# Optimization experiments

Hardware: AMD Instinct MI355X
Metric: run time of the kernel (lower is better)

## Reference

```python
import jax, jax.numpy as jnp
import numpy as np

B, L, C_IN, N_STOCKS = 128, 256, 8, 50
EPS = 1e-5
SIG_CH_1 = 14 + 14**2 + 14**3   # 2954 = signature_channels(14, 3)
SIG_CH_2 = 9 + 9**2 + 9**3      # 819  = signature_channels(9, 3)


def _conv1d(x, w, b):
    # x: (B, L, Cin); w: (Cout, Cin, K); 'valid' conv along the stream dim
    y = jax.lax.conv_general_dilated(x, w, window_strides=(1,), padding='VALID',
                                     dimension_numbers=('NWC', 'OIW', 'NWC'))
    return y + b


def _augment(x, convs, include_original, include_time):
    # signatory.Augment: conv stack (kernel K then kernel-1 convs with ReLU in between),
    # optionally concatenated with the truncated original stream and a time channel.
    K = convs[0][0].shape[-1]
    L_out = x.shape[1] - K + 1
    pieces = []
    if include_original:
        pieces.append(x[:, K - 1:, :])
    if include_time:
        t = jnp.linspace(0.0, 1.0, L_out, dtype=x.dtype)
        pieces.append(jnp.broadcast_to(t[None, :, None], (x.shape[0], L_out, 1)))
    h = _conv1d(x, *convs[0])
    for w, b in convs[1:]:
        h = _conv1d(jax.nn.relu(h), w, b)
    pieces.append(h)
    return jnp.concatenate(pieces, axis=2)


def _exp3(v):
    # truncated tensor-algebra exponential of a linear increment v: (B, C)
    l1 = v
    l2 = 0.5 * (v[:, :, None] * v[:, None, :])
    l3 = (v[:, :, None, None] * v[:, None, :, None] * v[:, None, None, :]) * (1.0 / 6.0)
    return l1, l2, l3


def _chen(a, b):
    # Chen's identity: truncated tensor product of two depth-3 signatures
    a1, a2, a3 = a
    b1, b2, b3 = b
    c1 = a1 + b1
    c2 = a2 + b2 + a1[:, :, None] * b1[:, None, :]
    c3 = (a3 + b3 + a1[:, :, None, None] * b2[:, None, :, :]
          + a2[:, :, :, None] * b1[:, None, None, :])
    return c1, c2, c3


def _flat(s):
    l1, l2, l3 = s
    bsz = l1.shape[0]
    return jnp.concatenate([l1, l2.reshape(bsz, -1), l3.reshape(bsz, -1)], axis=1)


def _signature(path, stream):
    # path: (B, L, C) -> depth-3 signature; stream=True returns sig at every step
    dx = path[:, 1:, :] - path[:, :-1, :]      # (B, S, C) increments
    init = _exp3(dx[:, 0])
    xs = jnp.moveaxis(dx[:, 1:, :], 1, 0)      # (S-1, B, C)

    def step(carry, v):
        new = _chen(carry, _exp3(v))
        return new, (_flat(new) if stream else jnp.float32(0.0))

    last, outs = jax.lax.scan(step, init, xs)
    if stream:
        return jnp.concatenate([_flat(init)[:, None, :], jnp.moveaxis(outs, 0, 1)], axis=1)
    return _flat(last)


def setup_inputs() -> dict:
    key = jax.random.key(0)
    ks = jax.random.split(key, 12)
    inp = {
        'x': jax.random.normal(ks[0], (B, L, C_IN), dtype=jnp.float32),
        'bn_gamma': jnp.ones((L,), jnp.float32),
        'bn_beta': jnp.zeros((L,), jnp.float32),
        'a1_w1': 0.05 * jax.random.normal(ks[1], (10, C_IN, 5), jnp.float32),
        'a1_b1': 0.05 * jax.random.normal(ks[2], (10,), jnp.float32),
        'a1_w2': 0.05 * jax.random.normal(ks[3], (5, 10, 1), jnp.float32),
        'a1_b2': 0.05 * jax.random.normal(ks[4], (5,), jnp.float32),
        'a2_w1': 0.005 * jax.random.normal(ks[5], (64, SIG_CH_1, 5), jnp.float32),
        'a2_b1': 0.05 * jax.random.normal(ks[6], (64,), jnp.float32),
        'a2_w2': 0.05 * jax.random.normal(ks[7], (8, 64, 1), jnp.float32),
        'a2_b2': 0.05 * jax.random.normal(ks[8], (8,), jnp.float32),
        'lin_w': 1e-4 * jax.random.normal(ks[9], (N_STOCKS, SIG_CH_2), jnp.float32),
        'lin_b': 1e-4 * jax.random.normal(ks[10], (N_STOCKS,), jnp.float32),
    }
    return inp


def reference(x, bn_gamma, bn_beta, a1_w1, a1_b1, a1_w2, a1_b2,
              a2_w1, a2_b1, a2_w2, a2_b2, lin_w, lin_b):
    # BatchNorm1d(nb_sequence) in training mode: normalize over (batch, channel) dims
    mean = x.mean(axis=(0, 2), keepdims=True)
    var = x.var(axis=(0, 2), keepdims=True)
    h = (x - mean) / jnp.sqrt(var + EPS) * bn_gamma[None, :, None] + bn_beta[None, :, None]
    h = _augment(h, [(a1_w1, a1_b1), (a1_w2, a1_b2)], include_original=True, include_time=True)
    h = _signature(h, stream=True)     # (B, L-5, 2954)
    h = _augment(h, [(a2_w1, a2_b1), (a2_w2, a2_b2)], include_original=False, include_time=True)
    h = _signature(h, stream=False)    # (B, 819)
    out = h @ lin_w.T + lin_b
    return jax.nn.softmax(out, axis=1)
```

## Files before the change

### kernel.cpp

```cpp
#include <hip/hip_runtime.h>
#include <cstdint>
#include <cstddef>


#define BATCH 128
#define LSEQ  256
#define CIN   8
#define L1P   252
#define NS1   251
#define SC1   2954
#define TOUT  247
#define OCH   64
#define SC2   819
#define NSTK  50
#define KFLAT 14770
#define KP    14784
#define NKCH  231

typedef __attribute__((ext_vector_type(8))) short short8;
typedef __attribute__((ext_vector_type(16))) float f32x16;

__device__ __forceinline__ void split8(float4 p, float4 q, uint4& hi, uint4& lo) {
  unsigned u0 = __float_as_uint(p.x), u1 = __float_as_uint(p.y);
  unsigned u2 = __float_as_uint(p.z), u3 = __float_as_uint(p.w);
  unsigned u4 = __float_as_uint(q.x), u5 = __float_as_uint(q.y);
  unsigned u6 = __float_as_uint(q.z), u7 = __float_as_uint(q.w);
  hi.x = __builtin_amdgcn_perm(u1, u0, 0x07060302u);
  hi.y = __builtin_amdgcn_perm(u3, u2, 0x07060302u);
  hi.z = __builtin_amdgcn_perm(u5, u4, 0x07060302u);
  hi.w = __builtin_amdgcn_perm(u7, u6, 0x07060302u);
  float r0 = p.x - __uint_as_float(u0 & 0xFFFF0000u);
  float r1 = p.y - __uint_as_float(u1 & 0xFFFF0000u);
  float r2 = p.z - __uint_as_float(u2 & 0xFFFF0000u);
  float r3 = p.w - __uint_as_float(u3 & 0xFFFF0000u);
  float r4 = q.x - __uint_as_float(u4 & 0xFFFF0000u);
  float r5 = q.y - __uint_as_float(u5 & 0xFFFF0000u);
  float r6 = q.z - __uint_as_float(u6 & 0xFFFF0000u);
  float r7 = q.w - __uint_as_float(u7 & 0xFFFF0000u);
  lo.x = __builtin_amdgcn_perm(__float_as_uint(r1), __float_as_uint(r0), 0x07060302u);
  lo.y = __builtin_amdgcn_perm(__float_as_uint(r3), __float_as_uint(r2), 0x07060302u);
  lo.z = __builtin_amdgcn_perm(__float_as_uint(r5), __float_as_uint(r4), 0x07060302u);
  lo.w = __builtin_amdgcn_perm(__float_as_uint(r7), __float_as_uint(r6), 0x07060302u);
}

__global__ __launch_bounds__(256) void k_bn(const float* __restrict__ x,
                                            const float* __restrict__ gamma,
                                            const float* __restrict__ beta,
                                            float* __restrict__ scale,
                                            float* __restrict__ shift) {
  int l = blockIdx.x, tid = threadIdx.x;
  float s = 0.f, q = 0.f;
#pragma unroll
  for (int p = 0; p < 4; ++p) {
    int e = tid + p * 256;
    int b = e >> 3, c = e & 7;
    float v = x[((size_t)b * LSEQ + l) * CIN + c];
    s += v; q += v * v;
  }
  for (int d = 32; d; d >>= 1) { s += __shfl_xor(s, d); q += __shfl_xor(q, d); }
  __shared__ float ss[4], qq[4];
  int w = tid >> 6;
  if ((tid & 63) == 0) { ss[w] = s; qq[w] = q; }
  __syncthreads();
  if (tid == 0) {
    float S = ss[0] + ss[1] + ss[2] + ss[3];
    float Q = qq[0] + qq[1] + qq[2] + qq[3];
    float mean = S * (1.f / 1024.f);
    float var  = Q * (1.f / 1024.f) - mean * mean;
    float istd = 1.0f / sqrtf(var + 1e-5f);
    float sc = istd * gamma[l];
    scale[l] = sc;
    shift[l] = beta[l] - mean * sc;
  }
}

__global__ __launch_bounds__(256) void k_aug1(const float* __restrict__ x,
                                              const float* __restrict__ scale,
                                              const float* __restrict__ shift,
                                              const float* __restrict__ w1,
                                              const float* __restrict__ b1,
                                              const float* __restrict__ w2,
                                              const float* __restrict__ b2,
                                              float* __restrict__ P1) {
  __shared__ float w1s[400], b1s[10], w2s[50], b2s[5];
  int tid = threadIdx.x;
  for (int i = tid; i < 400; i += 256) w1s[i] = w1[i];
  if (tid < 10) b1s[tid] = b1[tid];
  if (tid < 50) w2s[tid] = w2[tid];
  if (tid < 5)  b2s[tid] = b2[tid];
  __syncthreads();
  int g = blockIdx.x * 256 + tid;
  if (g >= BATCH * L1P) return;
  int b = g / L1P, t = g % L1P;
  float xn[5][8];
#pragma unroll
  for (int k = 0; k < 5; ++k) {
    int l = t + k;
    float sc = scale[l], sh = shift[l];
#pragma unroll
    for (int c = 0; c < 8; ++c)
      xn[k][c] = x[((size_t)b * LSEQ + l) * CIN + c] * sc + sh;
  }
  float r10[10];
#pragma unroll
  for (int co = 0; co < 10; ++co) {
    float s = b1s[co];
#pragma unroll
    for (int c = 0; c < 8; ++c)
#pragma unroll
      for (int k = 0; k < 5; ++k)
        s += xn[k][c] * w1s[co * 40 + c * 5 + k];
    r10[co] = fmaxf(s, 0.f);
  }
  float* o = P1 + ((size_t)b * L1P + t) * 14;
#pragma unroll
  for (int c = 0; c < 8; ++c) o[c] = xn[4][c];
  o[8] = (float)t * (1.0f / 251.0f);
#pragma unroll
  for (int oo = 0; oo < 5; ++oo) {
    float s = b2s[oo];
#pragma unroll
    for (int co = 0; co < 10; ++co) s += r10[co] * w2s[oo * 10 + co];
    o[9 + oo] = s;
  }
}

__global__ __launch_bounds__(256) void k_wtf(const float* __restrict__ w,
                                             float* __restrict__ Wf) {
  int idx = blockIdx.x * 256 + threadIdx.x;
  if (idx >= OCH * KP) return;
  int o = idx / KP, kf = idx % KP;
  float v = 0.f;
  if (kf < KFLAT) {
    int tap = kf / SC1, c = kf % SC1;
    v = w[((size_t)o * SC1 + c) * 5 + tap];
  }
  Wf[idx] = v;
}

__global__ __launch_bounds__(256) void k_scanA(const float* __restrict__ P1,
                                               float* __restrict__ Sw,
                                               int NRbuf, int w0, int RW) {
  int s = blockIdx.x, b = blockIdx.y, tid = threadIdx.x;
  int r0 = s * 16;
  int cnt = RW - r0; if (cnt > 16) cnt = 16;
  if (cnt <= 0) return;
  const float* p = P1 + (size_t)b * L1P * 14 + (size_t)(w0 + r0) * 14;
  float* Sb = Sw + ((size_t)b * NRbuf + r0) * SC1;
  __shared__ float a1s[14], a2s[196], vs[2][14], b2s[2][196];
  float a3[11];
  int ia[11], i2[11], il2[11], ik[11];
#pragma unroll
  for (int n = 0; n < 11; ++n) {
    int e = tid + n * 256;
    ia[n] = e / 196; i2[n] = e / 14; il2[n] = e % 196; ik[n] = e % 14;
  }
  if (tid < 14) vs[0][tid] = p[14 + tid] - p[tid];
  if (tid < 196) {
    int j = tid / 14, k = tid % 14;
    b2s[0][tid] = 0.5f * (p[14 + j] - p[j]) * (p[14 + k] - p[k]);
  }
  __syncthreads();
  for (int j = 0; j < cnt; ++j) {
    int buf = j & 1;
    float c1n = 0.f, c2n = 0.f;
    if (j == 0) {
      if (tid < 14)  c1n = vs[buf][tid];
      if (tid < 196) c2n = b2s[buf][tid];
#pragma unroll
      for (int n = 0; n < 11; ++n) {
        int e = tid + n * 256;
        if (e < 2744) a3[n] = vs[buf][ia[n]] * b2s[buf][il2[n]] * (1.f / 3.f);
      }
    } else {
#pragma unroll
      for (int n = 0; n < 11; ++n) {
        int e = tid + n * 256;
        if (e < 2744)
          a3[n] += (a1s[ia[n]] + vs[buf][ia[n]] * (1.f / 3.f)) * b2s[buf][il2[n]]
                 + a2s[i2[n]] * vs[buf][ik[n]];
      }
      if (tid < 196) c2n = a2s[tid] + b2s[buf][tid] + a1s[tid / 14] * vs[buf][tid % 14];
      if (tid < 14)  c1n = a1s[tid] + vs[buf][tid];
    }
    __syncthreads();
    if (tid < 14)  a1s[tid] = c1n;
    if (tid < 196) a2s[tid] = c2n;
    {
      float* o = Sb + (size_t)j * SC1;
      if (tid < 14)  o[tid] = c1n;
      if (tid < 196) o[14 + tid] = c2n;
#pragma unroll
      for (int n = 0; n < 11; ++n) {
        int e = tid + n * 256;
        if (e < 2744) o[210 + e] = a3[n];
      }
    }
    if (j + 1 < cnt) {
      int nb = buf ^ 1;
      const float* pj = p + (size_t)(j + 1) * 14;
      if (tid < 14) vs[nb][tid] = pj[14 + tid] - pj[tid];
      if (tid < 196) {
        int jj = tid / 14, kk = tid % 14;
        b2s[nb][tid] = 0.5f * (pj[14 + jj] - pj[jj]) * (pj[14 + kk] - pj[kk]);
      }
    }
    __syncthreads();
  }
}

__global__ __launch_bounds__(256) void k_scanB(const float* __restrict__ Sw,
                                               float* __restrict__ Pfx,
                                               float* __restrict__ carry,
                                               int NRbuf, int RW, int NC, int NCC) {
  int b = blockIdx.x, tid = threadIdx.x;
  __shared__ float a1s[14], a2s[196], b1s[14], b2s[196];
  float a3[11], b3[11];
  int ia[11], i2[11], il2[11], ik[11];
#pragma unroll
  for (int n = 0; n < 11; ++n) {
    int e = tid + n * 256;
    ia[n] = e / 196; i2[n] = e / 14; il2[n] = e % 196; ik[n] = e % 14;
  }
  const float* Sb = Sw + (size_t)b * NRbuf * SC1;
  float* cb = carry + (size_t)b * SC1;
  if (tid < 14)  a1s[tid] = cb[tid];
  if (tid < 196) a2s[tid] = cb[14 + tid];
#pragma unroll
  for (int n = 0; n < 11; ++n) { int e = tid + n * 256; if (e < 2744) a3[n] = cb[210 + e]; }
  __syncthreads();
  for (int s = 0; s < NC; ++s) {
    int cnt = RW - s * 16; if (cnt > 16) cnt = 16;
    const float* tr = Sb + (size_t)(s * 16 + cnt - 1) * SC1;
    if (tid < 14)  b1s[tid] = tr[tid];
    if (tid < 196) b2s[tid] = tr[14 + tid];
#pragma unroll
    for (int n = 0; n < 11; ++n) { int e = tid + n * 256; if (e < 2744) b3[n] = tr[210 + e]; }
    __syncthreads();
    float* ps = Pfx + ((size_t)b * 16 + s) * SC1;
    if (tid < 14)  ps[tid] = a1s[tid];
    if (tid < 196) ps[14 + tid] = a2s[tid];
#pragma unroll
    for (int n = 0; n < 11; ++n) { int e = tid + n * 256; if (e < 2744) ps[210 + e] = a3[n]; }
#pragma unroll
    for (int n = 0; n < 11; ++n) {
      int e = tid + n * 256;
      if (e < 2744) a3[n] += b3[n] + a1s[ia[n]] * b2s[il2[n]] + a2s[i2[n]] * b1s[ik[n]];
    }
    float c1n = 0.f, c2n = 0.f;
    if (tid < 196) c2n = a2s[tid] + b2s[tid] + a1s[tid / 14] * b1s[tid % 14];
    if (tid < 14)  c1n = a1s[tid] + b1s[tid];
    __syncthreads();
    if (tid < 14)  a1s[tid] = c1n;
    if (tid < 196) a2s[tid] = c2n;
    if (s == NCC - 1) {
      if (tid < 14)  cb[tid] = c1n;
      if (tid < 196) cb[14 + tid] = c2n;
#pragma unroll
      for (int n = 0; n < 11; ++n) { int e = tid + n * 256; if (e < 2744) cb[210 + e] = a3[n]; }
    }
  }
}

__global__ __launch_bounds__(256) void k_scanC3(float* __restrict__ Sw,
                                                const float* __restrict__ Pfx,
                                                int NRbuf, int RW) {
  int s = blockIdx.x, b = blockIdx.y, tid = threadIdx.x;
  int r0 = s * 16;
  int rows = RW - r0; if (rows > 16) rows = 16;
  if (rows <= 0) return;
  __shared__ float pa[SC1];
  __shared__ float lb[4][216];
  const float* P = Pfx + ((size_t)b * 16 + s) * SC1;
  for (int i = tid; i < SC1; i += 256) pa[i] = P[i];
  __syncthreads();
  int w = tid >> 6, lane = tid & 63;
  float* base = Sw + ((size_t)b * NRbuf + r0) * SC1;
#pragma unroll
  for (int j = 0; j < 4; ++j) {
    int rr = w + j * 4;
    if (rr < rows) {
      float* row = base + (size_t)rr * SC1;
      if (lane < 53) {
        float4 v = *(const float4*)(row + lane * 4);
        *(float4*)&lb[w][lane * 4] = v;
      }
      asm volatile("s_waitcnt lgkmcnt(0)" ::: "memory");
      for (int c = lane; c < SC1; c += 64) {
        float v = row[c];
        float f;
        if (c < 14) {
          f = pa[c] + v;
        } else if (c < 210) {
          int e = c - 14;
          f = pa[c] + v + pa[e / 14] * lb[w][e % 14];
        } else {
          int e = c - 210;
          int i3 = e / 196, rjk = e - i3 * 196;
          int i2 = e / 14,  kk  = e - i2 * 14;
          f = pa[c] + v + pa[i3] * lb[w][14 + rjk] + pa[14 + i2] * lb[w][kk];
        }
        row[c] = f;
      }
    }
  }
}

__global__ __launch_bounds__(256) void k_gemm3(const float* __restrict__ Sw,
                                               const float* __restrict__ Wf,
                                               const float* __restrict__ bias,
                                               float* __restrict__ C1,
                                               int NRbuf, int w0, int WTcur) {
  const int t0 = blockIdx.x * 64;
  const int b  = blockIdx.y;
  const int tid = threadIdx.x, lane = tid & 63;
  __shared__ __align__(16) short Ah[4096], Al[4096], Bh[4096], Bl[4096];
  f32x16 acc;
#pragma unroll
  for (int i = 0; i < 16; ++i) acc[i] = 0.f;

  const float* Sb = Sw + (size_t)b * ((size_t)NRbuf * SC1);
  const int arow = tid >> 2;
  const int g0 = tid & 3, g1 = g0 + 4;
  const int at = min(t0 + arow, WTcur - 1);
  const float* aP = Sb + (size_t)at * SC1;
  const float* bP = Wf + (size_t)arow * KP;
  const int sw = arow & 7;
  const int offA0 = arow * 64 + ((g0 ^ sw) << 3);
  const int offA1 = arow * 64 + ((g1 ^ sw) << 3);
  float4 a0, a1, a2, a3, w0v, w1v, w2v, w3v;

  auto LOADCH = [&](int k0) {
    a0 = *(const float4*)(aP + k0 + g0 * 8);
    a1 = *(const float4*)(aP + k0 + g0 * 8 + 4);
    a2 = *(const float4*)(aP + k0 + g1 * 8);
    a3 = *(const float4*)(aP + k0 + g1 * 8 + 4);
    w0v = *(const float4*)(bP + k0 + g0 * 8);
    w1v = *(const float4*)(bP + k0 + g0 * 8 + 4);
    w2v = *(const float4*)(bP + k0 + g1 * 8);
    w3v = *(const float4*)(bP + k0 + g1 * 8 + 4);
  };
  auto STORECH = [&]() {
    uint4 hi, lo;
    split8(a0, a1, hi, lo);
    *(uint4*)&Ah[offA0] = hi; *(uint4*)&Al[offA0] = lo;
    split8(a2, a3, hi, lo);
    *(uint4*)&Ah[offA1] = hi; *(uint4*)&Al[offA1] = lo;
    split8(w0v, w1v, hi, lo);
    *(uint4*)&Bh[offA0] = hi; *(uint4*)&Bl[offA0] = lo;
    split8(w2v, w3v, hi, lo);
    *(uint4*)&Bh[offA1] = hi; *(uint4*)&Bl[offA1] = lo;
  };

  const int rowA = ((tid >> 6) & 1) * 32 + (lane & 31);
  const int rowB = (tid >> 7) * 32 + (lane & 31);
  const int swA = rowA & 7, swB = rowB & 7;
  const int baseA = rowA * 64, baseB = rowB * 64;

  LOADCH(0);
  STORECH();
  __syncthreads();

  for (int ch = 0; ch < NKCH; ++ch) {
    if (ch + 1 < NKCH) LOADCH((ch + 1) * 64);
#pragma unroll
    for (int ks = 0; ks < 4; ++ks) {
      const int kga = 2 * ks + (lane >> 5);
      const short8 ah = *(const short8*)&Ah[baseA + ((kga ^ swA) << 3)];
      const short8 al = *(const short8*)&Al[baseA + ((kga ^ swA) << 3)];
      const short8 bh = *(const short8*)&Bh[baseB + ((kga ^ swB) << 3)];
      const short8 bl = *(const short8*)&Bl[baseB + ((kga ^ swB) << 3)];
      acc = __builtin_amdgcn_mfma_f32_32x32x16_bf16(ah, bh, acc, 0, 0, 0);
      acc = __builtin_amdgcn_mfma_f32_32x32x16_bf16(ah, bl, acc, 0, 0, 0);
      acc = __builtin_amdgcn_mfma_f32_32x32x16_bf16(al, bh, acc, 0, 0, 0);
    }
    __syncthreads();
    if (ch + 1 < NKCH) { STORECH(); __syncthreads(); }
  }

  const float bia = bias[rowB];
  const int mbase = t0 + ((tid >> 6) & 1) * 32;
#pragma unroll
  for (int q = 0; q < 16; ++q) {
    int crow = (q & 3) + 8 * (q >> 2) + 4 * (lane >> 5);
    int t_l = mbase + crow;
    if (t_l < WTcur)
      C1[((size_t)b * TOUT + w0 + t_l) * OCH + rowB] = acc[q] + bia;
  }
}

__global__ __launch_bounds__(256) void k_p2(const float* __restrict__ C1,
                                            const float* __restrict__ w2,
                                            const float* __restrict__ b2,
                                            float* __restrict__ P2) {
  int warp = blockIdx.x * 4 + (threadIdx.x >> 6);
  int lane = threadIdx.x & 63;
  int b = warp / TOUT, t = warp % TOUT;
  float v = fmaxf(C1[((size_t)b * TOUT + t) * OCH + lane], 0.f);
  float* o = P2 + ((size_t)b * TOUT + t) * 9;
#pragma unroll
  for (int oo = 0; oo < 8; ++oo) {
    float s = v * w2[oo * 64 + lane];
    for (int d = 32; d; d >>= 1) s += __shfl_xor(s, d);
    if (lane == oo) o[1 + oo] = s + b2[oo];
  }
  if (lane == 8) o[0] = (float)t * (1.0f / 246.0f);
}

__global__ __launch_bounds__(256) void k_sig2A(const float* __restrict__ P2,
                                               float* __restrict__ T2) {
  int ch = blockIdx.x, b = blockIdx.y, tid = threadIdx.x;
  int r0 = ch * 16;
  int steps = 246 - r0; if (steps > 16) steps = 16;
  const float* p = P2 + (size_t)b * TOUT * 9;
  __shared__ float a1s[9], a2s[81], vs[2][9], b2s[2][81];
  float a3[3];
  int ia[3], i2[3], il2[3], ik[3];
#pragma unroll
  for (int n = 0; n < 3; ++n) {
    int e = tid + n * 256;
    ia[n] = e / 81; i2[n] = e / 9; il2[n] = e % 81; ik[n] = e % 9;
  }
  {
    int r = r0;
    if (tid < 9) vs[0][tid] = p[(r + 1) * 9 + tid] - p[r * 9 + tid];
    if (tid < 81) {
      int j = tid / 9, k = tid % 9;
      b2s[0][tid] = 0.5f * (p[(r + 1) * 9 + j] - p[r * 9 + j])
                         * (p[(r + 1) * 9 + k] - p[r * 9 + k]);
    }
  }
  __syncthreads();
  for (int s = 0; s < steps; ++s) {
    int buf = s & 1, r = r0 + s;
    float c1n = 0.f, c2n = 0.f;
    if (s == 0) {
      if (tid < 9)  c1n = vs[buf][tid];
      if (tid < 81) c2n = b2s[buf][tid];
#pragma unroll
      for (int n = 0; n < 3; ++n) {
        int e = tid + n * 256;
        if (e < 729) a3[n] = vs[buf][ia[n]] * b2s[buf][il2[n]] * (1.f / 3.f);
      }
    } else {
#pragma unroll
      for (int n = 0; n < 3; ++n) {
        int e = tid + n * 256;
        if (e < 729)
          a3[n] += (a1s[ia[n]] + vs[buf][ia[n]] * (1.f / 3.f)) * b2s[buf][il2[n]]
                 + a2s[i2[n]] * vs[buf][ik[n]];
      }
      if (tid < 81) c2n = a2s[tid] + b2s[buf][tid] + a1s[tid / 9] * vs[buf][tid % 9];
      if (tid < 9)  c1n = a1s[tid] + vs[buf][tid];
    }
    __syncthreads();
    if (tid < 9)  a1s[tid] = c1n;
    if (tid < 81) a2s[tid] = c2n;
    if (s + 1 < steps) {
      int r2 = r + 1, nb = buf ^ 1;
      if (tid < 9) vs[nb][tid] = p[(r2 + 1) * 9 + tid] - p[r2 * 9 + tid];
      if (tid < 81) {
        int j = tid / 9, k = tid % 9;
        b2s[nb][tid] = 0.5f * (p[(r2 + 1) * 9 + j] - p[r2 * 9 + j])
                            * (p[(r2 + 1) * 9 + k] - p[r2 * 9 + k]);
      }
    }
    __syncthreads();
  }
  {
    float* tb = T2 + ((size_t)b * 16 + ch) * SC2;
    if (tid < 9)  tb[tid] = a1s[tid];
    if (tid < 81) tb[9 + tid] = a2s[tid];
#pragma unroll
    for (int n = 0; n < 3; ++n) {
      int e = tid + n * 256;
      if (e < 729) tb[90 + e] = a3[n];
    }
  }
}

__global__ __launch_bounds__(256) void k_sig2B(const float* __restrict__ T2,
                                               float* __restrict__ sg) {
  int b = blockIdx.x, tid = threadIdx.x;
  __shared__ float a1s[9], a2s[81], b1s[9], b2s[81];
  float a3[3], b3[3];
  int ia[3], i2[3], il2[3], ik[3];
#pragma unroll
  for (int n = 0; n < 3; ++n) {
    int e = tid + n * 256;
    ia[n] = e / 81; i2[n] = e / 9; il2[n] = e % 81; ik[n] = e % 9;
  }
  const float* base = T2 + (size_t)b * 16 * SC2;
  if (tid < 9)  a1s[tid] = base[tid];
  if (tid < 81) a2s[tid] = base[9 + tid];
#pragma unroll
  for (int n = 0; n < 3; ++n) { int e = tid + n * 256; if (e < 729) a3[n] = base[90 + e]; }
  __syncthreads();
  for (int ch = 1; ch < 16; ++ch) {
    const float* sl = base + (size_t)ch * SC2;
    if (tid < 9)  b1s[tid] = sl[tid];
    if (tid < 81) b2s[tid] = sl[9 + tid];
#pragma unroll
    for (int n = 0; n < 3; ++n) { int e = tid + n * 256; if (e < 729) b3[n] = sl[90 + e]; }
    __syncthreads();
#pragma unroll
    for (int n = 0; n < 3; ++n) {
      int e = tid + n * 256;
      if (e < 729) a3[n] += b3[n] + a1s[ia[n]] * b2s[il2[n]] + a2s[i2[n]] * b1s[ik[n]];
    }
    float c1n = 0.f, c2n = 0.f;
    if (tid < 81) c2n = a2s[tid] + b2s[tid] + a1s[tid / 9] * b1s[tid % 9];
    if (tid < 9)  c1n = a1s[tid] + b1s[tid];
    __syncthreads();
    if (tid < 9)  a1s[tid] = c1n;
    if (tid < 81) a2s[tid] = c2n;
    __syncthreads();
  }
  float* o = sg + (size_t)b * SC2;
  if (tid < 9)  o[tid] = a1s[tid];
  if (tid < 81) o[9 + tid] = a2s[tid];
#pragma unroll
  for (int n = 0; n < 3; ++n) { int e = tid + n * 256; if (e < 729) o[90 + e] = a3[n]; }
}

__global__ __launch_bounds__(64) void k_final(const float* __restrict__ sg,
                                              const float* __restrict__ lw,
                                              const float* __restrict__ lb,
                                              float* __restrict__ out) {
  int b = blockIdx.x, lane = threadIdx.x;
  float logit = -3.402823466e38f;
  if (lane < NSTK) {
    float s = lb[lane];
    const float* w = lw + (size_t)lane * SC2;
    const float* g = sg + (size_t)b * SC2;
    for (int c = 0; c < SC2; ++c) s += g[c] * w[c];
    logit = s;
  }
  float m = logit;
  for (int d = 32; d; d >>= 1) m = fmaxf(m, __shfl_xor(m, d));
  float e = (lane < NSTK) ? expf(logit - m) : 0.f;
  float sum = e;
  for (int d = 32; d; d >>= 1) sum += __shfl_xor(sum, d);
  if (lane < NSTK) out[(size_t)b * NSTK + lane] = e / sum;
}

extern "C" void kernel_launch(void* const* d_in, const int* in_sizes, int n_in,
                              void* d_out, int out_size, void* d_ws, size_t ws_size,
                              hipStream_t stream) {
  const float* x      = (const float*)d_in[0];
  const float* gamma  = (const float*)d_in[1];
  const float* beta   = (const float*)d_in[2];
  const float* a1w1   = (const float*)d_in[3];
  const float* a1b1   = (const float*)d_in[4];
  const float* a1w2   = (const float*)d_in[5];
  const float* a1b2   = (const float*)d_in[6];
  const float* a2w1   = (const float*)d_in[7];
  const float* a2b1   = (const float*)d_in[8];
  const float* a2w2   = (const float*)d_in[9];
  const float* a2b2   = (const float*)d_in[10];
  const float* lin_w  = (const float*)d_in[11];
  const float* lin_b  = (const float*)d_in[12];
  float* out = (float*)d_out;

  float* ws = (float*)d_ws;
  float* scale = ws;
  float* shift = ws + 256;
  float* P1    = ws + 512;
  float* Wf    = ws + 452096;
  float* carry = ws + 1398272;
  float* Pfx   = ws + 1776384;
  float* P2    = ws + 7826176;
  float* sig2  = ws + 8110720;
  float* C1    = ws + 8215552;
  const size_t off_Swin = 10238976;
  float* Swin  = ws + off_Swin;
  float* T2    = Pfx;

  size_t ws_floats = ws_size / 4;
  long avail = (long)ws_floats - (long)off_Swin - 64;
  long slot = (long)BATCH * SC1;
  int NRbuf = (int)(avail > 0 ? avail / slot : 0);
  if (NRbuf > 251) NRbuf = 251;
  if (NRbuf < 24)  NRbuf = 24;
  int WT = (NRbuf >= 251) ? 247 : ((NRbuf - 4) / 16) * 16;
  int nwin = (TOUT + WT - 1) / WT;

  hipMemsetAsync(carry, 0, (size_t)slot * 4, stream);

  k_bn  <<<LSEQ, 256, 0, stream>>>(x, gamma, beta, scale, shift);
  k_aug1<<<(BATCH * L1P) / 256, 256, 0, stream>>>(x, scale, shift, a1w1, a1b1, a1w2, a1b2, P1);
  k_wtf <<<(OCH * KP) / 256, 256, 0, stream>>>(a2w1, Wf);

  for (int w = 0; w < nwin; ++w) {
    int w0 = w * WT;
    int WTcur = TOUT - w0; if (WTcur > WT) WTcur = WT;
    int RW = WTcur + 4;
    int NC = (RW + 15) / 16;
    int NCC = (w + 1 < nwin) ? (WT / 16) : -2;
    k_scanA<<<dim3(NC, BATCH), 256, 0, stream>>>(P1, Swin, NRbuf, w0, RW);
    k_scanB<<<BATCH, 256, 0, stream>>>(Swin, Pfx, carry, NRbuf, RW, NC, NCC);
    k_scanC3<<<dim3(NC, BATCH), 256, 0, stream>>>(Swin, Pfx, NRbuf, RW);
    int tiles = (WTcur + 63) / 64;
    k_gemm3<<<dim3(tiles, BATCH), 256, 0, stream>>>(Swin, Wf, a2b1, C1, NRbuf, w0, WTcur);
  }

  k_p2   <<<(BATCH * TOUT) / 4, 256, 0, stream>>>(C1, a2w2, a2b2, P2);
  k_sig2A<<<dim3(16, BATCH), 256, 0, stream>>>(P2, T2);
  k_sig2B<<<BATCH, 256, 0, stream>>>(T2, sig2);
  k_final<<<BATCH, 64, 0, stream>>>(sig2, lin_w, lin_b, out);
}
```

Measured before the change: 1.144 ms.

## Pre-pack bf16 hi/lo pairs, use 128x64 tiles with split-K GEMM

The scan epilogue and the weight transform now store each float as a packed 32-bit word holding a bf16 high part and a rounded bf16 residual. The GEMM no longer has to split fp32 into hi/lo inside its loop, and each operand occupies one shared-memory array instead of two. The GEMM is rewritten to use 128x64 tiles with two accumulators per wave and split-K across blocks, writing partial sums that k_p2 reduces and adds the bias to. This is meant to raise parallelism and per-tile reuse, at the cost of extra partial-sum traffic and a larger workspace, which may shrink the window buffer.

```diff
diff --git a/kernel.cpp b/kernel.cpp
--- a/kernel.cpp
+++ b/kernel.cpp
@@ -20,27 +20,13 @@
 typedef __attribute__((ext_vector_type(8))) short short8;
 typedef __attribute__((ext_vector_type(16))) float f32x16;
 
-__device__ __forceinline__ void split8(float4 p, float4 q, uint4& hi, uint4& lo) {
-  unsigned u0 = __float_as_uint(p.x), u1 = __float_as_uint(p.y);
-  unsigned u2 = __float_as_uint(p.z), u3 = __float_as_uint(p.w);
-  unsigned u4 = __float_as_uint(q.x), u5 = __float_as_uint(q.y);
-  unsigned u6 = __float_as_uint(q.z), u7 = __float_as_uint(q.w);
-  hi.x = __builtin_amdgcn_perm(u1, u0, 0x07060302u);
-  hi.y = __builtin_amdgcn_perm(u3, u2, 0x07060302u);
-  hi.z = __builtin_amdgcn_perm(u5, u4, 0x07060302u);
-  hi.w = __builtin_amdgcn_perm(u7, u6, 0x07060302u);
-  float r0 = p.x - __uint_as_float(u0 & 0xFFFF0000u);
-  float r1 = p.y - __uint_as_float(u1 & 0xFFFF0000u);
-  float r2 = p.z - __uint_as_float(u2 & 0xFFFF0000u);
-  float r3 = p.w - __uint_as_float(u3 & 0xFFFF0000u);
-  float r4 = q.x - __uint_as_float(u4 & 0xFFFF0000u);
-  float r5 = q.y - __uint_as_float(u5 & 0xFFFF0000u);
-  float r6 = q.z - __uint_as_float(u6 & 0xFFFF0000u);
-  float r7 = q.w - __uint_as_float(u7 & 0xFFFF0000u);
-  lo.x = __builtin_amdgcn_perm(__float_as_uint(r1), __float_as_uint(r0), 0x07060302u);
-  lo.y = __builtin_amdgcn_perm(__float_as_uint(r3), __float_as_uint(r2), 0x07060302u);
-  lo.z = __builtin_amdgcn_perm(__float_as_uint(r5), __float_as_uint(r4), 0x07060302u);
-  lo.w = __builtin_amdgcn_perm(__float_as_uint(r7), __float_as_uint(r6), 0x07060302u);
+__device__ __forceinline__ unsigned int pack2(float x) {
+  unsigned int u = __float_as_uint(x);
+  unsigned int hi = u >> 16;
+  float rem = x - __uint_as_float(hi << 16);
+  unsigned int v = __float_as_uint(rem);
+  unsigned int lo = (v + 0x7FFFu + ((v >> 16) & 1u)) >> 16;
+  return (hi << 16) | lo;
 }
 
 __global__ __launch_bounds__(256) void k_bn(const float* __restrict__ x,
@@ -125,8 +111,8 @@
   }
 }
 
-__global__ __launch_bounds__(256) void k_wtf(const float* __restrict__ w,
-                                             float* __restrict__ Wf) {
+__global__ __launch_bounds__(256) void k_wtp(const float* __restrict__ w,
+                                             unsigned int* __restrict__ Wp) {
   int idx = blockIdx.x * 256 + threadIdx.x;
   if (idx >= OCH * KP) return;
   int o = idx / KP, kf = idx % KP;
@@ -135,7 +121,7 @@
     int tap = kf / SC1, c = kf % SC1;
     v = w[((size_t)o * SC1 + c) * 5 + tap];
   }
-  Wf[idx] = v;
+  Wp[idx] = pack2(v);
 }
 
 __global__ __launch_bounds__(256) void k_scanA(const float* __restrict__ P1,
@@ -281,6 +267,7 @@
     int rr = w + j * 4;
     if (rr < rows) {
       float* row = base + (size_t)rr * SC1;
+      unsigned int* rowp = (unsigned int*)row;
       if (lane < 53) {
         float4 v = *(const float4*)(row + lane * 4);
         *(float4*)&lb[w][lane * 4] = v;
@@ -300,103 +287,144 @@
           int i2 = e / 14,  kk  = e - i2 * 14;
           f = pa[c] + v + pa[i3] * lb[w][14 + rjk] + pa[14 + i2] * lb[w][kk];
         }
-        row[c] = f;
-      }
-    }
-  }
-}
-
-__global__ __launch_bounds__(256) void k_gemm3(const float* __restrict__ Sw,
-                                               const float* __restrict__ Wf,
-                                               const float* __restrict__ bias,
-                                               float* __restrict__ C1,
-                                               int NRbuf, int w0, int WTcur) {
-  const int t0 = blockIdx.x * 64;
-  const int b  = blockIdx.y;
-  const int tid = threadIdx.x, lane = tid & 63;
-  __shared__ __align__(16) short Ah[4096], Al[4096], Bh[4096], Bl[4096];
-  f32x16 acc;
-#pragma unroll
-  for (int i = 0; i < 16; ++i) acc[i] = 0.f;
-
-  const float* Sb = Sw + (size_t)b * ((size_t)NRbuf * SC1);
-  const int arow = tid >> 2;
-  const int g0 = tid & 3, g1 = g0 + 4;
-  const int at = min(t0 + arow, WTcur - 1);
-  const float* aP = Sb + (size_t)at * SC1;
-  const float* bP = Wf + (size_t)arow * KP;
-  const int sw = arow & 7;
-  const int offA0 = arow * 64 + ((g0 ^ sw) << 3);
-  const int offA1 = arow * 64 + ((g1 ^ sw) << 3);
-  float4 a0, a1, a2, a3, w0v, w1v, w2v, w3v;
-
-  auto LOADCH = [&](int k0) {
-    a0 = *(const float4*)(aP + k0 + g0 * 8);
-    a1 = *(const float4*)(aP + k0 + g0 * 8 + 4);
-    a2 = *(const float4*)(aP + k0 + g1 * 8);
-    a3 = *(const float4*)(aP + k0 + g1 * 8 + 4);
-    w0v = *(const float4*)(bP + k0 + g0 * 8);
-    w1v = *(const float4*)(bP + k0 + g0 * 8 + 4);
-    w2v = *(const float4*)(bP + k0 + g1 * 8);
-    w3v = *(const float4*)(bP + k0 + g1 * 8 + 4);
+        rowp[c] = pack2(f);
+      }
+    }
+  }
+}
+
+__global__ __launch_bounds__(256, 3) void k_gemm4(const unsigned int* __restrict__ Sp,
+                                                  const unsigned int* __restrict__ Wp,
+                                                  float* __restrict__ Cpart,
+                                                  int NRbuf, int w0, int WTcur,
+                                                  int nks, int cpk) {
+  const int mt = blockIdx.x / nks, ksid = blockIdx.x % nks;
+  const int b = blockIdx.y;
+  const int tid = threadIdx.x, lane = tid & 63, w = tid >> 6;
+  __shared__ unsigned int As[128 * 64];
+  __shared__ unsigned int Bs[64 * 64];
+  f32x16 acc0, acc1;
+#pragma unroll
+  for (int i = 0; i < 16; ++i) { acc0[i] = 0.f; acc1[i] = 0.f; }
+
+  const unsigned int* Sb = Sp + (size_t)b * ((size_t)NRbuf * SC1);
+  const int slot = tid & 15;
+  const int rsub = (tid >> 4) & 3;
+  uint4 ra[8], rb[4];
+  const int c0 = ksid * cpk;
+  int c1 = c0 + cpk; if (c1 > NKCH) c1 = NKCH;
+
+  auto GLOAD = [&](int ch) {
+    const int k0 = ch * 64;
+#pragma unroll
+    for (int p = 0; p < 8; ++p) {
+      int rl = w * 32 + p * 4 + rsub;
+      int t = mt * 128 + rl; if (t > WTcur - 1) t = WTcur - 1;
+      ra[p] = *(const uint4*)(Sb + (size_t)t * SC1 + k0 + slot * 4);
+    }
+#pragma unroll
+    for (int p = 0; p < 4; ++p) {
+      int o = w * 16 + p * 4 + rsub;
+      rb[p] = *(const uint4*)(Wp + (size_t)o * KP + k0 + slot * 4);
+    }
   };
-  auto STORECH = [&]() {
-    uint4 hi, lo;
-    split8(a0, a1, hi, lo);
-    *(uint4*)&Ah[offA0] = hi; *(uint4*)&Al[offA0] = lo;
-    split8(a2, a3, hi, lo);
-    *(uint4*)&Ah[offA1] = hi; *(uint4*)&Al[offA1] = lo;
-    split8(w0v, w1v, hi, lo);
-    *(uint4*)&Bh[offA0] = hi; *(uint4*)&Bl[offA0] = lo;
-    split8(w2v, w3v, hi, lo);
-    *(uint4*)&Bh[offA1] = hi; *(uint4*)&Bl[offA1] = lo;
+  auto SSTORE = [&]() {
+#pragma unroll
+    for (int p = 0; p < 8; ++p) {
+      int rl = w * 32 + p * 4 + rsub;
+      *(uint4*)&As[rl * 64 + ((slot ^ (rl & 15)) << 2)] = ra[p];
+    }
+#pragma unroll
+    for (int p = 0; p < 4; ++p) {
+      int o = w * 16 + p * 4 + rsub;
+      *(uint4*)&Bs[o * 64 + ((slot ^ (o & 15)) << 2)] = rb[p];
+    }
   };
 
-  const int rowA = ((tid >> 6) & 1) * 32 + (lane & 31);
-  const int rowB = (tid >> 7) * 32 + (lane & 31);
-  const int swA = rowA & 7, swB = rowB & 7;
-  const int baseA = rowA * 64, baseB = rowB * 64;
-
-  LOADCH(0);
-  STORECH();
-  __syncthreads();
-
-  for (int ch = 0; ch < NKCH; ++ch) {
-    if (ch + 1 < NKCH) LOADCH((ch + 1) * 64);
+  GLOAD(c0);
+  SSTORE();
+  __syncthreads();
+
+  const int rA = w * 32 + (lane & 31);
+  const int cB0 = lane & 31, cB1 = cB0 + 32;
+  const int swA = rA & 15, swB = cB0 & 15;
+  const int hsh = (lane >> 5) << 1;
+
+  union U { unsigned int u[4]; short8 s; };
+
+  for (int ch = c0; ch < c1; ++ch) {
+    if (ch + 1 < c1) GLOAD(ch + 1);
 #pragma unroll
     for (int ks = 0; ks < 4; ++ks) {
-      const int kga = 2 * ks + (lane >> 5);
-      const short8 ah = *(const short8*)&Ah[baseA + ((kga ^ swA) << 3)];
-      const short8 al = *(const short8*)&Al[baseA + ((kga ^ swA) << 3)];
-      const short8 bh = *(const short8*)&Bh[baseB + ((kga ^ swB) << 3)];
-      const short8 bl = *(const short8*)&Bl[baseB + ((kga ^ swB) << 3)];
-      acc = __builtin_amdgcn_mfma_f32_32x32x16_bf16(ah, bh, acc, 0, 0, 0);
-      acc = __builtin_amdgcn_mfma_f32_32x32x16_bf16(ah, bl, acc, 0, 0, 0);
-      acc = __builtin_amdgcn_mfma_f32_32x32x16_bf16(al, bh, acc, 0, 0, 0);
-    }
-    __syncthreads();
-    if (ch + 1 < NKCH) { STORECH(); __syncthreads(); }
-  }
-
-  const float bia = bias[rowB];
-  const int mbase = t0 + ((tid >> 6) & 1) * 32;
+      const int s0 = ks * 4 + hsh;
+      const uint4 aA = *(const uint4*)&As[rA * 64 + ((s0 ^ swA) << 2)];
+      const uint4 aB = *(const uint4*)&As[rA * 64 + (((s0 + 1) ^ swA) << 2)];
+      const uint4 p0 = *(const uint4*)&Bs[cB0 * 64 + ((s0 ^ swB) << 2)];
+      const uint4 p1 = *(const uint4*)&Bs[cB0 * 64 + (((s0 + 1) ^ swB) << 2)];
+      const uint4 q0 = *(const uint4*)&Bs[cB1 * 64 + ((s0 ^ swB) << 2)];
+      const uint4 q1 = *(const uint4*)&Bs[cB1 * 64 + (((s0 + 1) ^ swB) << 2)];
+      U ah, al, b0h, b0l, b1h, b1l;
+      ah.u[0] = __builtin_amdgcn_perm(aA.y, aA.x, 0x07060302u);
+      ah.u[1] = __builtin_amdgcn_perm(aA.w, aA.z, 0x07060302u);
+      ah.u[2] = __builtin_amdgcn_perm(aB.y, aB.x, 0x07060302u);
+      ah.u[3] = __builtin_amdgcn_perm(aB.w, aB.z, 0x07060302u);
+      al.u[0] = __builtin_amdgcn_perm(aA.y, aA.x, 0x05040100u);
+      al.u[1] = __builtin_amdgcn_perm(aA.w, aA.z, 0x05040100u);
+      al.u[2] = __builtin_amdgcn_perm(aB.y, aB.x, 0x05040100u);
+      al.u[3] = __builtin_amdgcn_perm(aB.w, aB.z, 0x05040100u);
+      b0h.u[0] = __builtin_amdgcn_perm(p0.y, p0.x, 0x07060302u);
+      b0h.u[1] = __builtin_amdgcn_perm(p0.w, p0.z, 0x07060302u);
+      b0h.u[2] = __builtin_amdgcn_perm(p1.y, p1.x, 0x07060302u);
+      b0h.u[3] = __builtin_amdgcn_perm(p1.w, p1.z, 0x07060302u);
+      b0l.u[0] = __builtin_amdgcn_perm(p0.y, p0.x, 0x05040100u);
+      b0l.u[1] = __builtin_amdgcn_perm(p0.w, p0.z, 0x05040100u);
+      b0l.u[2] = __builtin_amdgcn_perm(p1.y, p1.x, 0x05040100u);
+      b0l.u[3] = __builtin_amdgcn_perm(p1.w, p1.z, 0x05040100u);
+      b1h.u[0] = __builtin_amdgcn_perm(q0.y, q0.x, 0x07060302u);
+      b1h.u[1] = __builtin_amdgcn_perm(q0.w, q0.z, 0x07060302u);
+      b1h.u[2] = __builtin_amdgcn_perm(q1.y, q1.x, 0x07060302u);
+      b1h.u[3] = __builtin_amdgcn_perm(q1.w, q1.z, 0x07060302u);
+      b1l.u[0] = __builtin_amdgcn_perm(q0.y, q0.x, 0x05040100u);
+      b1l.u[1] = __builtin_amdgcn_perm(q0.w, q0.z, 0x05040100u);
+      b1l.u[2] = __builtin_amdgcn_perm(q1.y, q1.x, 0x05040100u);
+      b1l.u[3] = __builtin_amdgcn_perm(q1.w, q1.z, 0x05040100u);
+      acc0 = __builtin_amdgcn_mfma_f32_32x32x16_bf16(ah.s, b0h.s, acc0, 0, 0, 0);
+      acc0 = __builtin_amdgcn_mfma_f32_32x32x16_bf16(ah.s, b0l.s, acc0, 0, 0, 0);
+      acc0 = __builtin_amdgcn_mfma_f32_32x32x16_bf16(al.s, b0h.s, acc0, 0, 0, 0);
+      acc1 = __builtin_amdgcn_mfma_f32_32x32x16_bf16(ah.s, b1h.s, acc1, 0, 0, 0);
+      acc1 = __builtin_amdgcn_mfma_f32_32x32x16_bf16(ah.s, b1l.s, acc1, 0, 0, 0);
+      acc1 = __builtin_amdgcn_mfma_f32_32x32x16_bf16(al.s, b1h.s, acc1, 0, 0, 0);
+    }
+    __syncthreads();
+    if (ch + 1 < c1) { SSTORE(); __syncthreads(); }
+  }
+
+  const size_t part = ((size_t)ksid * BATCH + b) * TOUT * OCH;
 #pragma unroll
   for (int q = 0; q < 16; ++q) {
     int crow = (q & 3) + 8 * (q >> 2) + 4 * (lane >> 5);
-    int t_l = mbase + crow;
-    if (t_l < WTcur)
-      C1[((size_t)b * TOUT + w0 + t_l) * OCH + rowB] = acc[q] + bia;
-  }
-}
-
-__global__ __launch_bounds__(256) void k_p2(const float* __restrict__ C1,
+    int tl = mt * 128 + w * 32 + crow;
+    if (tl < WTcur) {
+      size_t o = part + (size_t)(w0 + tl) * OCH;
+      Cpart[o + cB0] = acc0[q];
+      Cpart[o + cB1] = acc1[q];
+    }
+  }
+}
+
+__global__ __launch_bounds__(256) void k_p2(const float* __restrict__ Cpart,
+                                            const float* __restrict__ bias,
                                             const float* __restrict__ w2,
                                             const float* __restrict__ b2,
-                                            float* __restrict__ P2) {
+                                            float* __restrict__ P2, int nks) {
   int warp = blockIdx.x * 4 + (threadIdx.x >> 6);
   int lane = threadIdx.x & 63;
   int b = warp / TOUT, t = warp % TOUT;
-  float v = fmaxf(C1[((size_t)b * TOUT + t) * OCH + lane], 0.f);
+  size_t idx = ((size_t)b * TOUT + t) * OCH + lane;
+  const size_t part = (size_t)BATCH * TOUT * OCH;
+  float v = bias[lane];
+  for (int ks = 0; ks < nks; ++ks) v += Cpart[(size_t)ks * part + idx];
+  v = fmaxf(v, 0.f);
   float* o = P2 + ((size_t)b * TOUT + t) * 9;
 #pragma unroll
   for (int oo = 0; oo < 8; ++oo) {
@@ -563,33 +591,42 @@
   float* out = (float*)d_out;
 
   float* ws = (float*)d_ws;
-  float* scale = ws;
-  float* shift = ws + 256;
-  float* P1    = ws + 512;
-  float* Wf    = ws + 452096;
-  float* carry = ws + 1398272;
-  float* Pfx   = ws + 1776384;
-  float* P2    = ws + 7826176;
-  float* sig2  = ws + 8110720;
-  float* C1    = ws + 8215552;
-  const size_t off_Swin = 10238976;
-  float* Swin  = ws + off_Swin;
-  float* T2    = Pfx;
-
+  float*        scale = ws;
+  float*        shift = ws + 256;
+  float*        P1    = ws + 512;
+  unsigned int* Wp    = (unsigned int*)(ws + 452096);
+  float*        carry = ws + 1398272;
+  float*        Pfx   = ws + 1776384;
+  float*        P2    = ws + 7826176;
+  float*        sig2  = ws + 8110720;
+  float*        Cpart = ws + 8215552;
+  float*        T2    = Pfx;
+
+  const size_t PARTSZ = (size_t)BATCH * TOUT * OCH;
   size_t ws_floats = ws_size / 4;
-  long avail = (long)ws_floats - (long)off_Swin - 64;
   long slot = (long)BATCH * SC1;
+
+  int nks = 4;
+  long off_Swin = 0, avail = 0;
+  for (;;) {
+    off_Swin = 8215552 + (long)nks * (long)PARTSZ;
+    avail = (long)ws_floats - off_Swin - 1024;
+    if (nks == 1 || (avail > 0 && avail / slot >= 24)) break;
+    nks >>= 1;
+  }
   int NRbuf = (int)(avail > 0 ? avail / slot : 0);
   if (NRbuf > 251) NRbuf = 251;
   if (NRbuf < 24)  NRbuf = 24;
   int WT = (NRbuf >= 251) ? 247 : ((NRbuf - 4) / 16) * 16;
   int nwin = (TOUT + WT - 1) / WT;
+  int cpk = (NKCH + nks - 1) / nks;
+  float* Swin = ws + off_Swin;
 
   hipMemsetAsync(carry, 0, (size_t)slot * 4, stream);
 
   k_bn  <<<LSEQ, 256, 0, stream>>>(x, gamma, beta, scale, shift);
   k_aug1<<<(BATCH * L1P) / 256, 256, 0, stream>>>(x, scale, shift, a1w1, a1b1, a1w2, a1b2, P1);
-  k_wtf <<<(OCH * KP) / 256, 256, 0, stream>>>(a2w1, Wf);
+  k_wtp <<<(OCH * KP) / 256, 256, 0, stream>>>(a2w1, Wp);
 
   for (int w = 0; w < nwin; ++w) {
     int w0 = w * WT;
@@ -600,11 +637,12 @@
     k_scanA<<<dim3(NC, BATCH), 256, 0, stream>>>(P1, Swin, NRbuf, w0, RW);
     k_scanB<<<BATCH, 256, 0, stream>>>(Swin, Pfx, carry, NRbuf, RW, NC, NCC);
     k_scanC3<<<dim3(NC, BATCH), 256, 0, stream>>>(Swin, Pfx, NRbuf, RW);
-    int tiles = (WTcur + 63) / 64;
-    k_gemm3<<<dim3(tiles, BATCH), 256, 0, stream>>>(Swin, Wf, a2b1, C1, NRbuf, w0, WTcur);
-  }
-
-  k_p2   <<<(BATCH * TOUT) / 4, 256, 0, stream>>>(C1, a2w2, a2b2, P2);
+    int mtiles = (WTcur + 127) / 128;
+    k_gemm4<<<dim3(mtiles * nks, BATCH), 256, 0, stream>>>(
+        (const unsigned int*)Swin, Wp, Cpart, NRbuf, w0, WTcur, nks, cpk);
+  }
+
+  k_p2   <<<(BATCH * TOUT) / 4, 256, 0, stream>>>(Cpart, a2b1, a2w2, a2b2, P2, nks);
   k_sig2A<<<dim3(16, BATCH), 256, 0, stream>>>(P2, T2);
   k_sig2B<<<BATCH, 256, 0, stream>>>(T2, sig2);
   k_final<<<BATCH, 64, 0, stream>>>(sig2, lin_w, lin_b, out);
```

Measured after the change: 1.500 ms. 31.1% more time.
